# Kernel optimization log

Measured on AMD Instinct MI355X. Metric: run time of the kernel, lower is better.

Reference implementation:

```python
import jax, jax.numpy as jnp
import numpy as np

B, S, D_MODEL, N_HEADS, HIDDEN = 4, 2048, 1024, 16, 4096
D_HEAD = D_MODEL // N_HEADS
LN_EPS = 1e-5


def setup_inputs() -> dict:
    key = jax.random.key(0)
    ks = jax.random.split(key, 20)
    s = 0.02
    return {
        "X": jax.random.normal(ks[0], (B, S, D_MODEL), dtype=jnp.float32),
        # attention projections (stored [in, out]; y = x @ W + b)
        "Wq": jax.random.normal(ks[1], (D_MODEL, D_MODEL), dtype=jnp.float32) * s,
        "bq": jnp.zeros((D_MODEL,), jnp.float32),
        "Wk": jax.random.normal(ks[2], (D_MODEL, D_MODEL), dtype=jnp.float32) * s,
        "bk": jnp.zeros((D_MODEL,), jnp.float32),
        "Wv": jax.random.normal(ks[3], (D_MODEL, D_MODEL), dtype=jnp.float32) * s,
        "bv": jnp.zeros((D_MODEL,), jnp.float32),
        "Wo": jax.random.normal(ks[4], (D_MODEL, D_MODEL), dtype=jnp.float32) * s,
        "bo": jnp.zeros((D_MODEL,), jnp.float32),
        # layernorm 1
        "g1": jnp.ones((D_MODEL,), jnp.float32),
        "beta1": jnp.zeros((D_MODEL,), jnp.float32),
        # FFN
        "W1": jax.random.normal(ks[5], (D_MODEL, HIDDEN), dtype=jnp.float32) * s,
        "b1": jnp.zeros((HIDDEN,), jnp.float32),
        "W2": jax.random.normal(ks[6], (HIDDEN, D_MODEL), dtype=jnp.float32) * s,
        "b2": jnp.zeros((D_MODEL,), jnp.float32),
        # layernorm 2
        "g2": jnp.ones((D_MODEL,), jnp.float32),
        "beta2": jnp.zeros((D_MODEL,), jnp.float32),
    }


def _layer_norm(x, gamma, beta):
    mu = jnp.mean(x, axis=-1, keepdims=True)
    var = jnp.mean(jnp.square(x - mu), axis=-1, keepdims=True)
    return (x - mu) * jax.lax.rsqrt(var + LN_EPS) * gamma + beta


def reference(X, Wq, bq, Wk, bk, Wv, bv, Wo, bo, g1, beta1, W1, b1, W2, b2, g2, beta2):
    b, s, d = X.shape
    # multi-head attention (dropout is identity in eval mode)
    q = (X @ Wq + bq).reshape(b, s, N_HEADS, D_HEAD)
    k = (X @ Wk + bk).reshape(b, s, N_HEADS, D_HEAD)
    v = (X @ Wv + bv).reshape(b, s, N_HEADS, D_HEAD)
    scale = 1.0 / np.sqrt(D_HEAD).astype(np.float32)
    scores = jnp.einsum('bqhd,bkhd->bhqk', q, k) * scale
    attn = jax.nn.softmax(scores, axis=-1)
    ctx = jnp.einsum('bhqk,bkhd->bqhd', attn, v).reshape(b, s, d)
    attn_out = ctx @ Wo + bo
    # AddNorm 1
    Y = _layer_norm(X + attn_out, g1, beta1)
    # FFN
    ffn_out = jax.nn.relu(Y @ W1 + b1) @ W2 + b2
    # AddNorm 2
    return _layer_norm(Y + ffn_out, g2, beta2)
```

## Files before the change

### kernel.cpp

```cpp
#include <hip/hip_runtime.h>
#include <stdint.h>

typedef unsigned short u16;
typedef short bf16x8 __attribute__((ext_vector_type(8)));
typedef float f32x4 __attribute__((ext_vector_type(4)));
typedef float f32x16 __attribute__((ext_vector_type(16)));
typedef u16 u16x4 __attribute__((ext_vector_type(4)));
typedef u16 u16x8 __attribute__((ext_vector_type(8)));

#define LOG2E 1.4426950408889634f
#define QSCALE (0.125f * LOG2E)

__device__ __forceinline__ u16 f2bf(float f) {
  union { float f; uint32_t u; } x; x.f = f;
  uint32_t r = x.u + 0x7fffu + ((x.u >> 16) & 1u);
  return (u16)(r >> 16);
}
__device__ __forceinline__ u16 f2bf_ru(float f) {
  union { float f; uint32_t u; } x; x.f = f;
  return (u16)((x.u + 0x8000u) >> 16);
}
__device__ __forceinline__ float bf2f(u16 h) {
  union { uint32_t u; float f; } x; x.u = ((uint32_t)h) << 16;
  return x.f;
}
__device__ __forceinline__ uint32_t cvtpk(float lo, float hi) {
  uint32_t r;
  asm("v_cvt_pk_bf16_f32 %0, %1, %2" : "=v"(r) : "v"(lo), "v"(hi));
  return r;
}
__device__ __forceinline__ int swz3(int row) { return (row ^ (row >> 3)) & 7; }

__device__ __forceinline__ void gload_lds16(const void* g, void* lds) {
  __builtin_amdgcn_global_load_lds(
      (const __attribute__((address_space(1))) void*)g,
      (__attribute__((address_space(3))) void*)lds, 16, 0, 0);
}

__global__ __launch_bounds__(256) void cast_bf16(const float* __restrict__ in,
                                                 u16* __restrict__ out, int n8) {
  int i = blockIdx.x * 256 + threadIdx.x;
  const int stride = gridDim.x * 256;
  for (; i < n8; i += stride) {
    const f32x4* p = (const f32x4*)in + (size_t)i * 2;
    f32x4 a = p[0], b = p[1];
    u16x8 o;
    o[0] = f2bf(a[0]); o[1] = f2bf(a[1]); o[2] = f2bf(a[2]); o[3] = f2bf(a[3]);
    o[4] = f2bf(b[0]); o[5] = f2bf(b[1]); o[6] = f2bf(b[2]); o[7] = f2bf(b[3]);
    ((u16x8*)out)[i] = o;
  }
}

__global__ __launch_bounds__(256) void concat3(const float* __restrict__ a,
                                               const float* __restrict__ b,
                                               const float* __restrict__ c,
                                               float* __restrict__ o) {
  int i = blockIdx.x * 256 + threadIdx.x;
  if (i < 3072)
    o[i] = i < 1024 ? a[i] * QSCALE : (i < 2048 ? b[i - 1024] : c[i - 2048]);
}

__global__ __launch_bounds__(256) void transpose_cast(const float* __restrict__ in,
                                                      u16* __restrict__ out, int R, int C,
                                                      float scale) {
  __shared__ float tile[32][33];
  const int bc = blockIdx.x * 32, br = blockIdx.y * 32;
  const int tx = threadIdx.x & 31, ty = threadIdx.x >> 5;
#pragma unroll
  for (int i = 0; i < 32; i += 8)
    tile[ty + i][tx] = in[(size_t)(br + ty + i) * C + bc + tx];
  __syncthreads();
#pragma unroll
  for (int i = 0; i < 32; i += 8)
    out[(size_t)(bc + ty + i) * R + br + tx] = f2bf(tile[tx][ty + i] * scale);
}

__global__ __launch_bounds__(256) void vtrans(const u16* __restrict__ QKV,
                                              u16* __restrict__ Vtg) {
  __shared__ u16 tl[64][65];
  const int t = threadIdx.x;
  const int sblk = blockIdx.x, h = blockIdx.y, b = blockIdx.z;
  const int s0 = sblk * 64;
  const size_t ibase = ((size_t)b * 2048) * 3072 + 2048 + h * 64;
#pragma unroll
  for (int i = 0; i < 2; i++) {
    const int idx = i * 256 + t;
    const int sl = idx >> 3, d0 = (idx & 7) * 8;
    bf16x8 v = *(const bf16x8*)&QKV[ibase + (size_t)(s0 + sl) * 3072 + d0];
#pragma unroll
    for (int e = 0; e < 8; e++) tl[d0 + e][sl] = (u16)v[e];
  }
  __syncthreads();
  const size_t ob = ((size_t)(b * 16 + h) * 64) * 2048;
#pragma unroll
  for (int i = 0; i < 2; i++) {
    const int idx = i * 256 + t;
    const int r = idx >> 3, c0 = (idx & 7) * 8;
    u16x8 o;
#pragma unroll
    for (int e = 0; e < 8; e++) o[e] = tl[r][c0 + e];
    *(u16x8*)&Vtg[ob + (size_t)r * 2048 + s0 + c0] = o;
  }
}

template <int RELU>
__global__ __launch_bounds__(512, 2) void gemm8p(const u16* __restrict__ A,
                                                 const u16* __restrict__ BT,
                                                 const float* __restrict__ bias,
                                                 u16* __restrict__ Cb,
                                                 int M, int N, int K, int nbx) {
  __shared__ u16 As[2][256 * 64];
  __shared__ u16 Bs[2][256 * 64];
  const int t = threadIdx.x;
  const int w = t >> 6, lane = t & 63;
  const int l5 = lane & 31, hf = lane >> 5;
  const int wr = w >> 2, wc = w & 3;
  int bid = (int)blockIdx.x;
  const int cpx = (int)gridDim.x >> 3;
  bid = (bid & 7) * cpx + (bid >> 3);
  const int m0 = (bid / nbx) * 256, n0 = (bid % nbx) * 256;
  const int NT = K >> 6;
  const int row64 = t >> 3;
  const int colp = ((t & 7) ^ swz3(row64)) << 3;

#define STG_A(buf, tile, q) \
  gload_lds16(A + (size_t)(m0 + (q)*64 + row64) * K + ((tile) << 6) + colp, \
              &As[buf][(q)*4096 + w * 512])
#define STG_B(buf, tile, q) \
  gload_lds16(BT + (size_t)(n0 + (q)*64 + row64) * K + ((tile) << 6) + colp, \
              &Bs[buf][(q)*4096 + w * 512])
#define LDA32(dst, mfi, kb) { const int r_ = wr * 128 + (mfi)*32 + l5; \
  dst = *(const bf16x8*)&As[cur][r_ * 64 + (((((kb) << 1) + hf) ^ swz3(r_)) << 3)]; }
#define LDB32(dst, nfi, kb) { const int r_ = wc * 64 + (nfi)*32 + l5; \
  dst = *(const bf16x8*)&Bs[cur][r_ * 64 + (((((kb) << 1) + hf) ^ swz3(r_)) << 3)]; }
#define MFMA32(mh, nfi, barr) \
  __builtin_amdgcn_s_setprio(1); \
  _Pragma("unroll") for (int kb = 0; kb < 4; kb++) \
  _Pragma("unroll") for (int i = 0; i < 2; i++) \
    acc[((mh)*2 + i) * 2 + (nfi)] = __builtin_amdgcn_mfma_f32_32x32x16_bf16( \
        af[i][kb], barr[kb], acc[((mh)*2 + i) * 2 + (nfi)], 0, 0, 0); \
  __builtin_amdgcn_s_setprio(0);
#define BAR1() __builtin_amdgcn_s_barrier(); \
  asm volatile("s_waitcnt lgkmcnt(0)" ::: "memory"); \
  __builtin_amdgcn_sched_barrier(0)

  f32x16 acc[8];
#pragma unroll
  for (int i = 0; i < 8; i++)
#pragma unroll
    for (int j = 0; j < 16; j++) acc[i][j] = 0.f;

  STG_A(0, 0, 0); STG_A(0, 0, 2);
  STG_B(0, 0, 0); STG_B(0, 0, 1); STG_B(0, 0, 2); STG_B(0, 0, 3);
  STG_A(0, 0, 1); STG_A(0, 0, 3);
  asm volatile("s_waitcnt vmcnt(2)" ::: "memory");
  __builtin_amdgcn_s_barrier();

  for (int tile = 0; tile < NT; ++tile) {
    const int cur = tile & 1, nxt = cur ^ 1;
    const bool hn = (tile + 1) < NT;
    bf16x8 af[2][4], b0[4], b1[4];
#pragma unroll
    for (int kb = 0; kb < 4; kb++) { LDA32(af[0][kb], 0, kb); LDA32(af[1][kb], 1, kb); }
#pragma unroll
    for (int kb = 0; kb < 4; kb++) { LDB32(b0[kb], 0, kb); }
    if (hn) { STG_A(nxt, tile + 1, 0); STG_A(nxt, tile + 1, 2); }
    BAR1();
    MFMA32(0, 0, b0);
    __builtin_amdgcn_s_barrier();
#pragma unroll
    for (int kb = 0; kb < 4; kb++) { LDB32(b1[kb], 1, kb); }
    if (hn) { STG_B(nxt, tile + 1, 0); STG_B(nxt, tile + 1, 1); }
    BAR1();
    MFMA32(0, 1, b1);
    if (hn) { asm volatile("s_waitcnt vmcnt(4)" ::: "memory"); }
    else    { asm volatile("s_waitcnt vmcnt(0)" ::: "memory"); }
    __builtin_amdgcn_s_barrier();
#pragma unroll
    for (int kb = 0; kb < 4; kb++) { LDA32(af[0][kb], 2, kb); LDA32(af[1][kb], 3, kb); }
    if (hn) { STG_B(nxt, tile + 1, 2); STG_B(nxt, tile + 1, 3); }
    BAR1();
    MFMA32(1, 0, b0);
    __builtin_amdgcn_s_barrier();
    if (hn) { STG_A(nxt, tile + 1, 1); STG_A(nxt, tile + 1, 3); }
    BAR1();
    MFMA32(1, 1, b1);
    if (hn) { asm volatile("s_waitcnt vmcnt(2)" ::: "memory"); }
    __builtin_amdgcn_s_barrier();
  }
#undef STG_A
#undef STG_B
#undef LDA32
#undef LDB32
#undef MFMA32
#undef BAR1

#pragma unroll
  for (int mf = 0; mf < 4; mf++) {
#pragma unroll
    for (int nf = 0; nf < 2; nf++) {
      const int c = n0 + wc * 64 + nf * 32 + l5;
      const float bv = bias[c];
#pragma unroll
      for (int reg = 0; reg < 16; reg++) {
        const int r = m0 + wr * 128 + mf * 32 + (reg & 3) + 8 * (reg >> 2) + 4 * hf;
        float v = acc[mf * 2 + nf][reg] + bv;
        if (RELU) v = fmaxf(v, 0.f);
        Cb[(size_t)r * N + c] = f2bf(v);
      }
    }
  }
}

template <int RELU>
__global__ __launch_bounds__(512, 2) void gemm8n(const u16* __restrict__ A,
                                                 const u16* __restrict__ BT,
                                                 const float* __restrict__ bias,
                                                 u16* __restrict__ Cb,
                                                 int M, int N, int K, int nbx) {
  __shared__ u16 As[2][128 * 64];
  __shared__ u16 Bs[2][256 * 64];
  const int t = threadIdx.x;
  const int w = t >> 6, lane = t & 63;
  const int la = lane & 15, lb = lane >> 4;
  const int wr = w >> 2, wc = w & 3;
  int bid = (int)blockIdx.x;
  const int cpx = (int)gridDim.x >> 3;
  bid = (bid & 7) * cpx + (bid >> 3);
  const int m0 = (bid / nbx) * 128, n0 = (bid % nbx) * 256;
  const int NT = K >> 6;
  const int rowA = t >> 3;
  const int colpA = ((t & 7) ^ swz3(rowA)) << 3;

#define STG_An(buf, tile, q) \
  gload_lds16(A + (size_t)(m0 + (q)*64 + rowA) * K + ((tile) << 6) + colpA, \
              &As[buf][(q)*4096 + t * 8])
#define STG_Bn(buf, tile, c, i) { \
  const int r32_ = (i)*64 + (t >> 3); \
  const int R_ = ((r32_ >> 5) << 6) + (c)*32 + (r32_ & 31); \
  const int cp_ = ((t & 7) ^ swz3(R_)) << 3; \
  gload_lds16(BT + (size_t)(n0 + R_) * K + ((tile) << 6) + cp_, \
              &Bs[buf][R_ * 64 + (t & 7) * 8]); }
#define LDAn(dst, mf, ks) { const int r_ = wr * 64 + (mf)*16 + la; \
  dst = *(const bf16x8*)&As[cur][r_ * 64 + (((((ks) << 2) + lb) ^ swz3(r_)) << 3)]; }
#define LDBn(dst, nf, ks) { const int r_ = wc * 64 + (nf)*16 + la; \
  dst = *(const bf16x8*)&Bs[cur][r_ * 64 + (((((ks) << 2) + lb) ^ swz3(r_)) << 3)]; }
#define MFMAn(nh, barr) \
  __builtin_amdgcn_s_setprio(1); \
  _Pragma("unroll") for (int ks = 0; ks < 2; ks++) \
  _Pragma("unroll") for (int i = 0; i < 4; i++) \
  _Pragma("unroll") for (int j = 0; j < 2; j++) \
    acc[i][(nh)*2 + j] = __builtin_amdgcn_mfma_f32_16x16x32_bf16( \
        af[i][ks], barr[j][ks], acc[i][(nh)*2 + j], 0, 0, 0); \
  __builtin_amdgcn_s_setprio(0);
#define BARn() __builtin_amdgcn_s_barrier(); \
  asm volatile("s_waitcnt lgkmcnt(0)" ::: "memory"); \
  __builtin_amdgcn_sched_barrier(0)

  f32x4 acc[4][4];
#pragma unroll
  for (int i = 0; i < 4; i++)
#pragma unroll
    for (int j = 0; j < 4; j++) acc[i][j] = (f32x4){0.f, 0.f, 0.f, 0.f};

  STG_Bn(0, 0, 0, 0); STG_Bn(0, 0, 0, 1); STG_An(0, 0, 0);
  STG_An(0, 0, 1); STG_Bn(0, 0, 1, 0); STG_Bn(0, 0, 1, 1);
  asm volatile("s_waitcnt vmcnt(0)" ::: "memory");
  __builtin_amdgcn_s_barrier();

  for (int tile = 0; tile < NT; ++tile) {
    const int cur = tile & 1, nxt = cur ^ 1;
    const bool hn = (tile + 1) < NT;
    bf16x8 af[4][2], b0[2][2], b1[2][2];
#pragma unroll
    for (int i = 0; i < 4; i++) { LDAn(af[i][0], i, 0); LDAn(af[i][1], i, 1); }
#pragma unroll
    for (int j = 0; j < 2; j++) { LDBn(b0[j][0], j, 0); LDBn(b0[j][1], j, 1); }
    if (hn) { STG_Bn(nxt, tile + 1, 0, 0); STG_Bn(nxt, tile + 1, 0, 1); STG_An(nxt, tile + 1, 0); }
    BARn();
    MFMAn(0, b0);
    if (hn) { asm volatile("s_waitcnt vmcnt(3)" ::: "memory"); }
    else    { asm volatile("s_waitcnt vmcnt(0)" ::: "memory"); }
    __builtin_amdgcn_s_barrier();
#pragma unroll
    for (int j = 0; j < 2; j++) { LDBn(b1[j][0], 2 + j, 0); LDBn(b1[j][1], 2 + j, 1); }
    if (hn) { STG_An(nxt, tile + 1, 1); STG_Bn(nxt, tile + 1, 1, 0); STG_Bn(nxt, tile + 1, 1, 1); }
    BARn();
    MFMAn(1, b1);
    if (hn) { asm volatile("s_waitcnt vmcnt(2)" ::: "memory"); }
    __builtin_amdgcn_s_barrier();
  }
#undef STG_An
#undef STG_Bn
#undef LDAn
#undef LDBn
#undef MFMAn
#undef BARn

#pragma unroll
  for (int mf = 0; mf < 4; mf++) {
    const int r = m0 + wr * 64 + mf * 16 + lb * 4;
#pragma unroll
    for (int nf = 0; nf < 4; nf++) {
      const int c = n0 + wc * 64 + nf * 16 + la;
      const float bv = bias[c];
#pragma unroll
      for (int rr = 0; rr < 4; rr++) {
        float v = acc[mf][nf][rr] + bv;
        if (RELU) v = fmaxf(v, 0.f);
        Cb[(size_t)(r + rr) * N + c] = f2bf(v);
      }
    }
  }
}

__global__ __launch_bounds__(256, 3) void attn_fwd(const u16* __restrict__ Qg,
                                                   const u16* __restrict__ Kg,
                                                   const u16* __restrict__ Vtg,
                                                   u16* __restrict__ Og, int LDM) {
  constexpr int S = 2048, DMO = 1024, NT = S / 64;
  __shared__ u16 Ks[2][64 * 64];
  __shared__ u16 Vt[2][64 * 64];
  const int t = threadIdx.x, w = t >> 6, lane = t & 63;
  const int l5 = lane & 31, hf = lane >> 5;
  const int qb = blockIdx.x, h = blockIdx.y, b = blockIdx.z;
  const size_t base = ((size_t)b * S) * LDM + h * 64;
  const size_t vbase = ((size_t)(b * 16 + h) * 64) * 2048;
  const size_t obase = ((size_t)b * S) * DMO + h * 64;
  const int qrow0 = qb * 128 + w * 32;

#define ATT_STAGE(buf, kt_) { \
  _Pragma("unroll") for (int i = 0; i < 2; i++) { \
    const int s = i * 256 + t; const int r = s >> 3; const int cg = s & 7; \
    gload_lds16(Kg + base + (size_t)((kt_) + r) * LDM + ((cg ^ swz3(r)) << 3), \
                &Ks[buf][s * 8]); } \
  _Pragma("unroll") for (int i = 0; i < 2; i++) { \
    const int s = i * 256 + t; const int r = s >> 3; const int cg = s & 7; \
    gload_lds16(Vtg + vbase + (size_t)r * 2048 + (kt_) + ((cg ^ swz3(r)) << 3), \
                &Vt[buf][s * 8]); } }

  bf16x8 qf[4];
#pragma unroll
  for (int kb = 0; kb < 4; kb++)
    qf[kb] = *(const bf16x8*)&Qg[base + (size_t)(qrow0 + l5) * LDM + kb * 16 + hf * 8];

  f32x16 accO0, accO1, accL;
#pragma unroll
  for (int i = 0; i < 16; i++) { accO0[i] = 0.f; accO1[i] = 0.f; accL[i] = 0.f; }
  float m = -1e30f;

  bf16x8 ones;
#pragma unroll
  for (int i = 0; i < 8; i++) ones[i] = (short)0x3F80;

  ATT_STAGE(0, 0);
  asm volatile("s_waitcnt vmcnt(0)" ::: "memory");
  __builtin_amdgcn_s_barrier();

  for (int kt = 0; kt < NT; ++kt) {
    const int cur = kt & 1;
    if (kt + 1 < NT) ATT_STAGE(cur ^ 1, (kt + 1) * 64);

    f32x16 st0, st1;
#pragma unroll
    for (int i = 0; i < 16; i++) { st0[i] = 0.f; st1[i] = 0.f; }
    __builtin_amdgcn_s_setprio(1);
#pragma unroll
    for (int kb = 0; kb < 4; kb++) {
      const int r0 = l5, r1 = 32 + l5;
      bf16x8 kf0 = *(const bf16x8*)&Ks[cur][r0 * 64 + (((hf + 2 * kb) ^ swz3(r0)) << 3)];
      bf16x8 kf1 = *(const bf16x8*)&Ks[cur][r1 * 64 + (((hf + 2 * kb) ^ swz3(r1)) << 3)];
      st0 = __builtin_amdgcn_mfma_f32_32x32x16_bf16(kf0, qf[kb], st0, 0, 0, 0);
      st1 = __builtin_amdgcn_mfma_f32_32x32x16_bf16(kf1, qf[kb], st1, 0, 0, 0);
    }
    __builtin_amdgcn_s_setprio(0);

    float tm[16];
#pragma unroll
    for (int i = 0; i < 8; i++) tm[i] = fmaxf(st0[2 * i], st0[2 * i + 1]);
#pragma unroll
    for (int i = 0; i < 8; i++) tm[8 + i] = fmaxf(st1[2 * i], st1[2 * i + 1]);
#pragma unroll
    for (int i = 0; i < 8; i++) tm[i] = fmaxf(tm[i], tm[i + 8]);
#pragma unroll
    for (int i = 0; i < 4; i++) tm[i] = fmaxf(tm[i], tm[i + 4]);
    tm[0] = fmaxf(tm[0], tm[2]);
    tm[1] = fmaxf(tm[1], tm[3]);
    float rm = fmaxf(tm[0], tm[1]);
    if (__any(rm > m + 8.0f)) {
      float ra = rm, rb = rm;
      asm volatile("v_permlane32_swap_b32 %0, %1" : "+v"(ra), "+v"(rb));
      rm = fmaxf(rm, fmaxf(ra, rb));
      const float mN = fmaxf(m, rm);
      const float al = exp2f(m - mN);
      m = mN;
#pragma unroll
      for (int r = 0; r < 16; r++) {
        const float alr = __shfl(al, (r & 3) + 8 * (r >> 2) + 4 * hf, 64);
        accO0[r] *= alr; accO1[r] *= alr; accL[r] *= alr;
      }
    }

    uint32_t pw0[8], pw1[8];
#pragma unroll
    for (int r2 = 0; r2 < 8; r2++) {
      pw0[r2] = cvtpk(exp2f(st0[2 * r2] - m), exp2f(st0[2 * r2 + 1] - m));
      pw1[r2] = cvtpk(exp2f(st1[2 * r2] - m), exp2f(st1[2 * r2 + 1] - m));
    }
    bf16x8 pf[4];
    {
      uint32_t a0 = pw0[0], b0v = pw0[2], a1 = pw0[1], b1v = pw0[3];
      asm volatile("v_permlane32_swap_b32 %0, %1" : "+v"(a0), "+v"(b0v));
      asm volatile("v_permlane32_swap_b32 %0, %1" : "+v"(a1), "+v"(b1v));
      union { uint32_t u[4]; bf16x8 v; } k;
      k.u[0] = a0; k.u[1] = a1; k.u[2] = b0v; k.u[3] = b1v; pf[0] = k.v;
      uint32_t c0 = pw0[4], d0 = pw0[6], c1 = pw0[5], d1 = pw0[7];
      asm volatile("v_permlane32_swap_b32 %0, %1" : "+v"(c0), "+v"(d0));
      asm volatile("v_permlane32_swap_b32 %0, %1" : "+v"(c1), "+v"(d1));
      k.u[0] = c0; k.u[1] = c1; k.u[2] = d0; k.u[3] = d1; pf[1] = k.v;
      uint32_t e0 = pw1[0], f0 = pw1[2], e1 = pw1[1], f1 = pw1[3];
      asm volatile("v_permlane32_swap_b32 %0, %1" : "+v"(e0), "+v"(f0));
      asm volatile("v_permlane32_swap_b32 %0, %1" : "+v"(e1), "+v"(f1));
      k.u[0] = e0; k.u[1] = e1; k.u[2] = f0; k.u[3] = f1; pf[2] = k.v;
      uint32_t g0 = pw1[4], h0 = pw1[6], g1 = pw1[5], h1 = pw1[7];
      asm volatile("v_permlane32_swap_b32 %0, %1" : "+v"(g0), "+v"(h0));
      asm volatile("v_permlane32_swap_b32 %0, %1" : "+v"(g1), "+v"(h1));
      k.u[0] = g0; k.u[1] = g1; k.u[2] = h0; k.u[3] = h1; pf[3] = k.v;
    }

    __builtin_amdgcn_s_setprio(1);
#pragma unroll
    for (int kb = 0; kb < 4; kb++) {
      const int r0 = l5, r1 = 32 + l5;
      bf16x8 vf0 = *(const bf16x8*)&Vt[cur][r0 * 64 + (((hf + 2 * kb) ^ swz3(r0)) << 3)];
      bf16x8 vf1 = *(const bf16x8*)&Vt[cur][r1 * 64 + (((hf + 2 * kb) ^ swz3(r1)) << 3)];
      accO0 = __builtin_amdgcn_mfma_f32_32x32x16_bf16(pf[kb], vf0, accO0, 0, 0, 0);
      accO1 = __builtin_amdgcn_mfma_f32_32x32x16_bf16(pf[kb], vf1, accO1, 0, 0, 0);
      accL  = __builtin_amdgcn_mfma_f32_32x32x16_bf16(pf[kb], ones, accL, 0, 0, 0);
    }
    __builtin_amdgcn_s_setprio(0);

    asm volatile("s_waitcnt vmcnt(0)" ::: "memory");
    __builtin_amdgcn_s_barrier();
  }
#undef ATT_STAGE

#pragma unroll
  for (int r = 0; r < 16; r++) {
    const float inv = 1.0f / accL[r];
    const int row = qrow0 + (r & 3) + 8 * (r >> 2) + 4 * hf;
    Og[obase + (size_t)row * DMO + l5]      = f2bf_ru(accO0[r] * inv);
    Og[obase + (size_t)row * DMO + 32 + l5] = f2bf_ru(accO1[r] * inv);
  }
}

template <int AF32, int OUTF32>
__global__ __launch_bounds__(256) void add_ln(const void* __restrict__ Ap,
                                              const u16* __restrict__ Bb,
                                              const float* __restrict__ g,
                                              const float* __restrict__ be,
                                              void* __restrict__ Yp) {
  constexpr int D = 1024;
  const int row = blockIdx.x, t = threadIdx.x;
  f32x4 a;
  if (AF32) {
    a = ((const f32x4*)((const float*)Ap + (size_t)row * D))[t];
  } else {
    u16x4 av = ((const u16x4*)((const u16*)Ap + (size_t)row * D))[t];
#pragma unroll
    for (int i = 0; i < 4; i++) a[i] = bf2f(av[i]);
  }
  u16x4 bv16 = ((const u16x4*)(Bb + (size_t)row * D))[t];
  f32x4 x;
#pragma unroll
  for (int i = 0; i < 4; i++) x[i] = a[i] + bf2f(bv16[i]);
  float s1 = x[0] + x[1] + x[2] + x[3];
  float s2 = x[0] * x[0] + x[1] * x[1] + x[2] * x[2] + x[3] * x[3];
#pragma unroll
  for (int off = 32; off > 0; off >>= 1) {
    s1 += __shfl_down(s1, off, 64);
    s2 += __shfl_down(s2, off, 64);
  }
  __shared__ float sm[8];
  const int w = t >> 6, lane = t & 63;
  if (lane == 0) { sm[w] = s1; sm[4 + w] = s2; }
  __syncthreads();
  s1 = sm[0] + sm[1] + sm[2] + sm[3];
  s2 = sm[4] + sm[5] + sm[6] + sm[7];
  const float mean = s1 * (1.0f / D);
  const float var = s2 * (1.0f / D) - mean * mean;
  const float rstd = rsqrtf(var + 1e-5f);
  const f32x4 gv = ((const f32x4*)g)[t];
  const f32x4 bv = ((const f32x4*)be)[t];
  f32x4 y;
#pragma unroll
  for (int i = 0; i < 4; i++) y[i] = (x[i] - mean) * rstd * gv[i] + bv[i];
  if (OUTF32) {
    ((f32x4*)((float*)Yp + (size_t)row * D))[t] = y;
  } else {
    u16x4 o;
#pragma unroll
    for (int i = 0; i < 4; i++) o[i] = f2bf(y[i]);
    ((u16x4*)((u16*)Yp + (size_t)row * D))[t] = o;
  }
}

extern "C" void kernel_launch(void* const* d_in, const int* in_sizes, int n_in,
                              void* d_out, int out_size, void* d_ws, size_t ws_size,
                              hipStream_t stream) {
  const float* X   = (const float*)d_in[0];
  const float* Wq  = (const float*)d_in[1];
  const float* bq  = (const float*)d_in[2];
  const float* Wk  = (const float*)d_in[3];
  const float* bk  = (const float*)d_in[4];
  const float* Wv  = (const float*)d_in[5];
  const float* bv  = (const float*)d_in[6];
  const float* Wo  = (const float*)d_in[7];
  const float* bo  = (const float*)d_in[8];
  const float* g1  = (const float*)d_in[9];
  const float* be1 = (const float*)d_in[10];
  const float* W1  = (const float*)d_in[11];
  const float* b1  = (const float*)d_in[12];
  const float* W2  = (const float*)d_in[13];
  const float* b2  = (const float*)d_in[14];
  const float* g2  = (const float*)d_in[15];
  const float* be2 = (const float*)d_in[16];

  const size_t MB = 1ull << 20;
  char* wsb = (char*)d_ws;
  u16*   WqkvT = (u16*)(wsb + 0 * MB);
  u16*   WoT   = (u16*)(wsb + 6 * MB);
  u16*   W1T   = (u16*)(wsb + 8 * MB);
  u16*   W2T   = (u16*)(wsb + 16 * MB);
  u16*   Xb    = (u16*)(wsb + 24 * MB);
  u16*   Ab    = (u16*)(wsb + 24 * MB);
  u16*   Fb    = (u16*)(wsb + 24 * MB);
  u16*   QKVb  = (u16*)(wsb + 40 * MB);
  u16*   Hb    = (u16*)(wsb + 40 * MB);
  float* bqkv  = (float*)(wsb + 88 * MB);
  u16*   Cx    = (u16*)(wsb + 88 * MB);
  u16*   Vt_g  = (u16*)(wsb + 104 * MB);
  u16*   Yb    = (u16*)(wsb + 104 * MB);
  (void)ws_size; (void)in_sizes; (void)n_in; (void)out_size;

  cast_bf16<<<2048, 256, 0, stream>>>(X, Xb, 8192 * 1024 / 8);
  concat3<<<12, 256, 0, stream>>>(bq, bk, bv, bqkv);
  transpose_cast<<<dim3(32, 32), 256, 0, stream>>>(Wq, WqkvT, 1024, 1024, QSCALE);
  transpose_cast<<<dim3(32, 32), 256, 0, stream>>>(Wk, WqkvT + 1024 * 1024, 1024, 1024, 1.0f);
  transpose_cast<<<dim3(32, 32), 256, 0, stream>>>(Wv, WqkvT + 2 * 1024 * 1024, 1024, 1024, 1.0f);
  transpose_cast<<<dim3(32, 32), 256, 0, stream>>>(Wo, WoT, 1024, 1024, 1.0f);
  transpose_cast<<<dim3(128, 32), 256, 0, stream>>>(W1, W1T, 1024, 4096, 1.0f);
  transpose_cast<<<dim3(32, 128), 256, 0, stream>>>(W2, W2T, 4096, 1024, 1.0f);

  gemm8p<0><<<384, 512, 0, stream>>>(Xb, WqkvT, bqkv, QKVb, 8192, 3072, 1024, 12);

  vtrans<<<dim3(32, 16, 4), 256, 0, stream>>>(QKVb, Vt_g);
  attn_fwd<<<dim3(16, 16, 4), 256, 0, stream>>>(QKVb, QKVb + 1024, Vt_g, Cx, 3072);

  gemm8n<0><<<256, 512, 0, stream>>>(Cx, WoT, bo, Ab, 8192, 1024, 1024, 4);
  add_ln<1, 0><<<8192, 256, 0, stream>>>(X, Ab, g1, be1, Yb);
  gemm8p<1><<<512, 512, 0, stream>>>(Yb, W1T, b1, Hb, 8192, 4096, 1024, 16);
  gemm8n<0><<<256, 512, 0, stream>>>(Hb, W2T, b2, Fb, 8192, 1024, 4096, 4);
  add_ln<0, 1><<<8192, 256, 0, stream>>>(Yb, Fb, g2, be2, d_out);
}
```

Before: 430.9 us.

## Switch gemm8n to 32x32x16 MFMA tiles and simplify attention row-max reduction

Rewrites the 128x256 GEMM kernel's inner loop to use 32x32x16 bf16 MFMA instructions instead of 16x16x32. Each wave now holds four 32x32 accumulators, and the LDS fragment loads and epilogue indexing are updated to match. The larger MFMA shape needs fewer instructions and fewer LDS fragment reads per unit of work, at the cost of a different register layout and output write pattern. In attention, the tree max reduction is replaced by a linear fmax chain, which lengthens the dependency chain but is simpler code.

```diff
diff --git a/kernel.cpp b/kernel.cpp
--- a/kernel.cpp
+++ b/kernel.cpp
@@ -222,7 +222,7 @@
   __shared__ u16 Bs[2][256 * 64];
   const int t = threadIdx.x;
   const int w = t >> 6, lane = t & 63;
-  const int la = lane & 15, lb = lane >> 4;
+  const int l5 = lane & 31, hf = lane >> 5;
   const int wr = w >> 2, wc = w & 3;
   int bid = (int)blockIdx.x;
   const int cpx = (int)gridDim.x >> 3;
@@ -241,27 +241,26 @@
   const int cp_ = ((t & 7) ^ swz3(R_)) << 3; \
   gload_lds16(BT + (size_t)(n0 + R_) * K + ((tile) << 6) + cp_, \
               &Bs[buf][R_ * 64 + (t & 7) * 8]); }
-#define LDAn(dst, mf, ks) { const int r_ = wr * 64 + (mf)*16 + la; \
-  dst = *(const bf16x8*)&As[cur][r_ * 64 + (((((ks) << 2) + lb) ^ swz3(r_)) << 3)]; }
-#define LDBn(dst, nf, ks) { const int r_ = wc * 64 + (nf)*16 + la; \
-  dst = *(const bf16x8*)&Bs[cur][r_ * 64 + (((((ks) << 2) + lb) ^ swz3(r_)) << 3)]; }
-#define MFMAn(nh, barr) \
+#define LDAn(dst, mfi, kb) { const int r_ = wr * 64 + (mfi)*32 + l5; \
+  dst = *(const bf16x8*)&As[cur][r_ * 64 + (((((kb) << 1) + hf) ^ swz3(r_)) << 3)]; }
+#define LDBn(dst, nfi, kb) { const int r_ = wc * 64 + (nfi)*32 + l5; \
+  dst = *(const bf16x8*)&Bs[cur][r_ * 64 + (((((kb) << 1) + hf) ^ swz3(r_)) << 3)]; }
+#define MFMAn(nfi, barr) \
   __builtin_amdgcn_s_setprio(1); \
-  _Pragma("unroll") for (int ks = 0; ks < 2; ks++) \
-  _Pragma("unroll") for (int i = 0; i < 4; i++) \
-  _Pragma("unroll") for (int j = 0; j < 2; j++) \
-    acc[i][(nh)*2 + j] = __builtin_amdgcn_mfma_f32_16x16x32_bf16( \
-        af[i][ks], barr[j][ks], acc[i][(nh)*2 + j], 0, 0, 0); \
+  _Pragma("unroll") for (int kb = 0; kb < 4; kb++) \
+  _Pragma("unroll") for (int i = 0; i < 2; i++) \
+    acc[i * 2 + (nfi)] = __builtin_amdgcn_mfma_f32_32x32x16_bf16( \
+        af[i][kb], barr[kb], acc[i * 2 + (nfi)], 0, 0, 0); \
   __builtin_amdgcn_s_setprio(0);
 #define BARn() __builtin_amdgcn_s_barrier(); \
   asm volatile("s_waitcnt lgkmcnt(0)" ::: "memory"); \
   __builtin_amdgcn_sched_barrier(0)
 
-  f32x4 acc[4][4];
+  f32x16 acc[4];
 #pragma unroll
   for (int i = 0; i < 4; i++)
 #pragma unroll
-    for (int j = 0; j < 4; j++) acc[i][j] = (f32x4){0.f, 0.f, 0.f, 0.f};
+    for (int j = 0; j < 16; j++) acc[i][j] = 0.f;
 
   STG_Bn(0, 0, 0, 0); STG_Bn(0, 0, 0, 1); STG_An(0, 0, 0);
   STG_An(0, 0, 1); STG_Bn(0, 0, 1, 0); STG_Bn(0, 0, 1, 1);
@@ -271,11 +270,11 @@
   for (int tile = 0; tile < NT; ++tile) {
     const int cur = tile & 1, nxt = cur ^ 1;
     const bool hn = (tile + 1) < NT;
-    bf16x8 af[4][2], b0[2][2], b1[2][2];
-#pragma unroll
-    for (int i = 0; i < 4; i++) { LDAn(af[i][0], i, 0); LDAn(af[i][1], i, 1); }
-#pragma unroll
-    for (int j = 0; j < 2; j++) { LDBn(b0[j][0], j, 0); LDBn(b0[j][1], j, 1); }
+    bf16x8 af[2][4], b0[4], b1[4];
+#pragma unroll
+    for (int kb = 0; kb < 4; kb++) { LDAn(af[0][kb], 0, kb); LDAn(af[1][kb], 1, kb); }
+#pragma unroll
+    for (int kb = 0; kb < 4; kb++) { LDBn(b0[kb], 0, kb); }
     if (hn) { STG_Bn(nxt, tile + 1, 0, 0); STG_Bn(nxt, tile + 1, 0, 1); STG_An(nxt, tile + 1, 0); }
     BARn();
     MFMAn(0, b0);
@@ -283,7 +282,7 @@
     else    { asm volatile("s_waitcnt vmcnt(0)" ::: "memory"); }
     __builtin_amdgcn_s_barrier();
 #pragma unroll
-    for (int j = 0; j < 2; j++) { LDBn(b1[j][0], 2 + j, 0); LDBn(b1[j][1], 2 + j, 1); }
+    for (int kb = 0; kb < 4; kb++) { LDBn(b1[kb], 1, kb); }
     if (hn) { STG_An(nxt, tile + 1, 1); STG_Bn(nxt, tile + 1, 1, 0); STG_Bn(nxt, tile + 1, 1, 1); }
     BARn();
     MFMAn(1, b1);
@@ -298,17 +297,17 @@
 #undef BARn
 
 #pragma unroll
-  for (int mf = 0; mf < 4; mf++) {
-    const int r = m0 + wr * 64 + mf * 16 + lb * 4;
-#pragma unroll
-    for (int nf = 0; nf < 4; nf++) {
-      const int c = n0 + wc * 64 + nf * 16 + la;
+  for (int mf = 0; mf < 2; mf++) {
+#pragma unroll
+    for (int nf = 0; nf < 2; nf++) {
+      const int c = n0 + wc * 64 + nf * 32 + l5;
       const float bv = bias[c];
 #pragma unroll
-      for (int rr = 0; rr < 4; rr++) {
-        float v = acc[mf][nf][rr] + bv;
+      for (int reg = 0; reg < 16; reg++) {
+        const int r = m0 + wr * 64 + mf * 32 + (reg & 3) + 8 * (reg >> 2) + 4 * hf;
+        float v = acc[mf * 2 + nf][reg] + bv;
         if (RELU) v = fmaxf(v, 0.f);
-        Cb[(size_t)(r + rr) * N + c] = f2bf(v);
+        Cb[(size_t)r * N + c] = f2bf(v);
       }
     }
   }
@@ -375,18 +374,11 @@
     }
     __builtin_amdgcn_s_setprio(0);
 
-    float tm[16];
-#pragma unroll
-    for (int i = 0; i < 8; i++) tm[i] = fmaxf(st0[2 * i], st0[2 * i + 1]);
-#pragma unroll
-    for (int i = 0; i < 8; i++) tm[8 + i] = fmaxf(st1[2 * i], st1[2 * i + 1]);
-#pragma unroll
-    for (int i = 0; i < 8; i++) tm[i] = fmaxf(tm[i], tm[i + 8]);
-#pragma unroll
-    for (int i = 0; i < 4; i++) tm[i] = fmaxf(tm[i], tm[i + 4]);
-    tm[0] = fmaxf(tm[0], tm[2]);
-    tm[1] = fmaxf(tm[1], tm[3]);
-    float rm = fmaxf(tm[0], tm[1]);
+    float rm = st0[0];
+#pragma unroll
+    for (int i = 1; i < 16; i++) rm = fmaxf(rm, st0[i]);
+#pragma unroll
+    for (int i = 0; i < 16; i++) rm = fmaxf(rm, st1[i]);
     if (__any(rm > m + 8.0f)) {
       float ra = rm, rb = rm;
       asm volatile("v_permlane32_swap_b32 %0, %1" : "+v"(ra), "+v"(rb));
```

Result: faster. 415.3 us (-3.6%).
